# Kernel tuning notes

Measured on AMD Instinct MI355X. Metric: run time of the kernel, lower is better.

The kernel has to match this reference:

```python
import jax, jax.numpy as jnp
import numpy as np

N, C, O, R, T, V = 128, 64, 64, 8, 128, 25  # batch, in_ch, out_ch, rel_ch, frames, joints
EPS = 1e-5


def _c1(x, w, b):
    # 1x1 conv2d over channel dim: x [n,i,t,v], w [o,i], b [o]
    return jnp.einsum('oi,nitv->notv', w, x) + b[None, :, None, None]


def _tconv(x, w):
    # temporal conv, kernel [3,1], pad [1,0]: x [n,c,t,1], w [o,i,3,1]
    return jax.lax.conv_general_dilated(
        x, w, window_strides=(1, 1), padding=((1, 1), (0, 0)),
        dimension_numbers=('NCHW', 'OIHW', 'NCHW'))


def setup_inputs() -> dict:
    key = jax.random.key(0)
    ks = jax.random.split(key, 16)
    d = {}
    d['x'] = jax.random.normal(ks[0], (N, C, T, V), jnp.float32)
    d['A'] = jax.random.normal(ks[1], (V, V), jnp.float32) * 0.1
    d['alpha'] = jnp.ones((1,), jnp.float32)
    s_c = 1.0 / np.sqrt(C)
    s_r = 1.0 / np.sqrt(R)
    d['w1'] = jax.random.normal(ks[2], (R, C), jnp.float32) * s_c
    d['b1'] = jnp.zeros((R,), jnp.float32)
    d['w2'] = jax.random.normal(ks[3], (R, C), jnp.float32) * s_c
    d['b2'] = jnp.zeros((R,), jnp.float32)
    d['w5'] = jax.random.normal(ks[4], (R, C), jnp.float32) * s_c
    d['b5'] = jnp.zeros((R,), jnp.float32)
    d['w3'] = jax.random.normal(ks[5], (O, R), jnp.float32) * s_r
    d['b3'] = jnp.zeros((O,), jnp.float32)
    d['w4'] = jax.random.normal(ks[6], (O, R), jnp.float32) * s_r
    d['b4'] = jnp.zeros((O,), jnp.float32)
    # RouteFuncMLP params (ratio=1, kernels=[3,3])
    d['g_w'] = jax.random.normal(ks[7], (R, R), jnp.float32) * s_r
    d['g_b'] = jnp.zeros((R,), jnp.float32)
    d['a_w'] = jax.random.normal(ks[8], (R, R, 3, 1), jnp.float32) * s_r
    d['a_b'] = jnp.zeros((R,), jnp.float32)
    d['bn_g'] = jnp.ones((R,), jnp.float32)
    d['bn_b'] = jnp.zeros((R,), jnp.float32)
    d['bn_rm'] = jnp.zeros((R,), jnp.float32)
    d['bn_rv'] = jnp.ones((R,), jnp.float32)
    # conv_rf.b is zero-init in torch (trivial gate); randomize small for a meaningful test
    d['rf_bw'] = jax.random.normal(ks[9], (R, R, 3, 1), jnp.float32) * 0.05
    return d


def reference(x, A, alpha, w1, b1, w2, b2, w5, b5, w3, b3, w4, b4,
              g_w, g_b, a_w, a_b, bn_g, bn_b, bn_rm, bn_rv, rf_bw):
    # x1, x2: 1x1 conv then mean over T  -> [N,R,V]
    x1 = _c1(x, w1, b1).mean(axis=2)
    x2 = _c1(x, w2, b2).mean(axis=2)
    x3 = _c1(x, w5, b5)  # [N,R,T,V]

    # RouteFuncMLP gating on x3
    g = x3.mean(axis=(2, 3), keepdims=True)          # global pool [N,R,1,1]
    p = x3.mean(axis=3, keepdims=True)               # pool over V [N,R,T,1]
    gg = _c1(g, g_w, g_b)                            # 1x1 conv on global pool
    h = _tconv(p + gg, a_w) + a_b[None, :, None, None]
    h = (h - bn_rm[None, :, None, None]) * (bn_g / jnp.sqrt(bn_rv + EPS))[None, :, None, None] + bn_b[None, :, None, None]
    h = jax.nn.relu(h)
    rf = _tconv(h, rf_bw) + 1.0                      # [N,R,T,1]

    x3 = _c1(x3 * rf, w3, b3)                        # [N,O,T,V]

    # relation tensor: broadcast diff + tanh -> [N,R,V,V]
    rel = jnp.tanh(x1[:, :, :, None] - x2[:, :, None, :])
    rel = _c1(rel, w4, b4) * alpha[0] + A[None, None]  # [N,O,V,V]

    # aggregation: out[n,c,t,u] = sum_v rel[n,c,u,v] * x3[n,c,t,v]
    out = jnp.einsum('ncuv,nctv->nctu', rel, x3)
    return out
```

## Files before the change

kernel.cpp:

```cpp
#include <hip/hip_runtime.h>

#define N_ 128
#define C_ 64
#define O_ 64
#define R_ 8
#define T_ 128
#define V_ 25
#define TV_ 3200
#define EPS_ 1e-5f
#define G_ 8

__global__ __launch_bounds__(256) void k1_colsum(const float* __restrict__ x,
                                                 float* __restrict__ S) {
    int ni = blockIdx.x;
    const float* xp = x + (size_t)ni * TV_;
    int tid = threadIdx.x;
    __shared__ float part[200];
    if (tid < 200) {
        float s = 0.f;
        #pragma unroll
        for (int k = 0; k < 16; ++k) s += xp[tid + 200 * k];
        part[tid] = s;
    }
    __syncthreads();
    if (tid < V_) {
        float t = 0.f;
        #pragma unroll
        for (int g = 0; g < 8; ++g) t += part[g * 25 + tid];
        S[ni * V_ + tid] = t;
    }
}

__global__ __launch_bounds__(256) void k3_x3(const float* __restrict__ x,
        const float* __restrict__ w5, const float* __restrict__ b5,
        float* __restrict__ x3) {
    int gid = blockIdx.x * 256 + threadIdx.x;
    int n = gid / TV_, p = gid % TV_;
    float acc[R_];
    #pragma unroll
    for (int r = 0; r < R_; ++r) acc[r] = b5[r];
    const float* xp = x + (size_t)n * C_ * TV_ + p;
    #pragma unroll
    for (int i = 0; i < C_; ++i) {
        float xv = xp[(size_t)i * TV_];
        #pragma unroll
        for (int r = 0; r < R_; ++r) acc[r] += w5[r * C_ + i] * xv;
    }
    float* x3p = x3 + (size_t)n * R_ * TV_ + p;
    #pragma unroll
    for (int r = 0; r < R_; ++r) x3p[(size_t)r * TV_] = acc[r];
}

__global__ __launch_bounds__(256) void k2_rel(const float* __restrict__ S,
        const float* __restrict__ w1, const float* __restrict__ b1,
        const float* __restrict__ w2, const float* __restrict__ b2,
        const float* __restrict__ w4, const float* __restrict__ b4,
        const float* __restrict__ A, const float* __restrict__ alpha,
        float* __restrict__ rel2) {
    int n = blockIdx.x, og = blockIdx.y;
    int c0 = og * 16;
    int tid = threadIdx.x;
    __shared__ float x1s[R_ * V_];
    __shared__ float x2s[R_ * V_];
    __shared__ float rels[R_ * 625];
    const float invT = 1.0f / (float)T_;
    for (int idx = tid; idx < 2 * R_ * V_; idx += 256) {
        int s = idx / (R_ * V_), rv = idx % (R_ * V_);
        int r = rv / V_, v = rv % V_;
        const float* w = s ? w2 : w1;
        float a = 0.f;
        for (int i = 0; i < C_; ++i) a += w[r * C_ + i] * S[(n * C_ + i) * V_ + v];
        a = a * invT + (s ? b2[r] : b1[r]);
        (s ? x2s : x1s)[rv] = a;
    }
    __syncthreads();
    for (int idx = tid; idx < R_ * 625; idx += 256) {
        int r = idx / 625, uv = idx % 625;
        rels[idx] = tanhf(x1s[r * V_ + uv / V_] - x2s[r * V_ + uv % V_]);
    }
    __syncthreads();
    float al = alpha[0];
    for (int idx = tid; idx < 16 * 625; idx += 256) {
        int o = c0 + idx / 625, uv = idx % 625;
        float acc = b4[o];
        #pragma unroll
        for (int r = 0; r < R_; ++r) acc += w4[o * R_ + r] * rels[r * 625 + uv];
        rel2[((size_t)n * O_ + o) * 625 + uv] = acc * al + A[uv];
    }
}

__global__ __launch_bounds__(256) void k4_route(const float* __restrict__ x3,
        const float* __restrict__ g_w, const float* __restrict__ g_b,
        const float* __restrict__ a_w, const float* __restrict__ a_b,
        const float* __restrict__ bn_g, const float* __restrict__ bn_b,
        const float* __restrict__ bn_rm, const float* __restrict__ bn_rv,
        const float* __restrict__ rf_bw, float* __restrict__ rf) {
    int n = blockIdx.x, tid = threadIdx.x;
    __shared__ float ps[R_][T_];
    __shared__ float hs[R_][T_];
    __shared__ float gs[R_];
    __shared__ float ggs[R_];
    for (int idx = tid; idx < R_ * T_; idx += 256) {
        int r = idx / T_, t = idx % T_;
        const float* xp = x3 + ((size_t)n * R_ + r) * TV_ + t * V_;
        float s = 0.f;
        #pragma unroll
        for (int v = 0; v < V_; ++v) s += xp[v];
        ps[r][t] = s * (1.0f / V_);
    }
    __syncthreads();
    if (tid < R_) {
        float s = 0.f;
        for (int t = 0; t < T_; ++t) s += ps[tid][t];
        gs[tid] = s * (1.0f / T_);
    }
    __syncthreads();
    if (tid < R_) {
        float a = g_b[tid];
        #pragma unroll
        for (int i = 0; i < R_; ++i) a += g_w[tid * R_ + i] * gs[i];
        ggs[tid] = a;
    }
    __syncthreads();
    for (int idx = tid; idx < R_ * T_; idx += 256) {
        int r = idx / T_, t = idx % T_;
        float acc = a_b[r];
        #pragma unroll
        for (int i = 0; i < R_; ++i) {
            #pragma unroll
            for (int k = 0; k < 3; ++k) {
                int tt = t + k - 1;
                if (tt >= 0 && tt < T_)
                    acc += a_w[(r * R_ + i) * 3 + k] * (ps[i][tt] + ggs[i]);
            }
        }
        float sc = bn_g[r] * rsqrtf(bn_rv[r] + EPS_);
        float h = (acc - bn_rm[r]) * sc + bn_b[r];
        hs[r][t] = fmaxf(h, 0.f);
    }
    __syncthreads();
    for (int idx = tid; idx < R_ * T_; idx += 256) {
        int r = idx / T_, t = idx % T_;
        float acc = 1.0f;
        #pragma unroll
        for (int i = 0; i < R_; ++i) {
            #pragma unroll
            for (int k = 0; k < 3; ++k) {
                int tt = t + k - 1;
                if (tt >= 0 && tt < T_)
                    acc += rf_bw[(r * R_ + i) * 3 + k] * hs[i][tt];
            }
        }
        rf[((size_t)n * R_ + r) * T_ + t] = acc;
    }
}

__global__ __launch_bounds__(512) void k5_out(const float* __restrict__ x3,
        const float* __restrict__ rf, const float* __restrict__ rel2,
        const float* __restrict__ w3, const float* __restrict__ b3,
        float* __restrict__ out) {
    int b = blockIdx.x;
    int n = b / 16;
    int rem = b % 16;
    int cg = rem / 2, th = rem % 2;
    int c0 = cg * G_;
    int tid = threadIdx.x;
    __shared__ float rfs[R_][64];
    __shared__ float zs[G_][1600];
    __shared__ float rels[G_][V_][28];
    if (tid < R_ * 64) {
        int r = tid / 64, tl = tid % 64;
        rfs[r][tl] = rf[((size_t)n * R_ + r) * T_ + th * 64 + tl];
    }
    for (int idx = tid; idx < G_ * 625; idx += 512) {
        int cl = idx / 625, uv = idx % 625;
        rels[cl][uv / 25][uv % 25] = rel2[((size_t)n * O_ + c0 + cl) * 625 + uv];
    }
    __syncthreads();
    const float* x3p = x3 + (size_t)n * R_ * TV_ + th * 1600;
    for (int p = tid; p < 1600; p += 512) {
        int t = p / V_;
        float y[R_];
        #pragma unroll
        for (int r = 0; r < R_; ++r) y[r] = x3p[(size_t)r * TV_ + p] * rfs[r][t];
        #pragma unroll
        for (int cl = 0; cl < G_; ++cl) {
            float a = b3[c0 + cl];
            #pragma unroll
            for (int r = 0; r < R_; ++r) a += w3[(c0 + cl) * R_ + r] * y[r];
            zs[cl][p] = a;
        }
    }
    __syncthreads();
    {
        int cl = tid >> 6, tl = tid & 63;
        float zreg[V_];
        #pragma unroll
        for (int v = 0; v < V_; ++v) zreg[v] = zs[cl][tl * V_ + v];
        float accu[V_];
        #pragma unroll
        for (int u = 0; u < V_; ++u) {
            const float4* rp4 = (const float4*)&rels[cl][u][0];
            float4 a0 = rp4[0], a1 = rp4[1], a2 = rp4[2];
            float4 a3 = rp4[3], a4 = rp4[4], a5 = rp4[5];
            float acc = zreg[24] * rels[cl][u][24];
            acc += zreg[0] * a0.x + zreg[1] * a0.y + zreg[2] * a0.z + zreg[3] * a0.w;
            acc += zreg[4] * a1.x + zreg[5] * a1.y + zreg[6] * a1.z + zreg[7] * a1.w;
            acc += zreg[8] * a2.x + zreg[9] * a2.y + zreg[10] * a2.z + zreg[11] * a2.w;
            acc += zreg[12] * a3.x + zreg[13] * a3.y + zreg[14] * a3.z + zreg[15] * a3.w;
            acc += zreg[16] * a4.x + zreg[17] * a4.y + zreg[18] * a4.z + zreg[19] * a4.w;
            acc += zreg[20] * a5.x + zreg[21] * a5.y + zreg[22] * a5.z + zreg[23] * a5.w;
            accu[u] = acc;
        }
        #pragma unroll
        for (int u = 0; u < V_; ++u) zs[cl][tl * V_ + u] = accu[u];
    }
    __syncthreads();
    size_t ob = (((size_t)n * O_ + c0) * T_ + th * 64) * V_;
    const float* zf = &zs[0][0];
    for (int j = tid; j < G_ * 1600; j += 512) {
        int cl = j / 1600, rest = j % 1600;
        out[ob + (size_t)cl * (T_ * V_) + rest] = zf[j];
    }
}

extern "C" void kernel_launch(void* const* d_in, const int* in_sizes, int n_in,
                              void* d_out, int out_size, void* d_ws, size_t ws_size,
                              hipStream_t stream) {
    const float* x     = (const float*)d_in[0];
    const float* A     = (const float*)d_in[1];
    const float* alpha = (const float*)d_in[2];
    const float* w1    = (const float*)d_in[3];
    const float* b1    = (const float*)d_in[4];
    const float* w2    = (const float*)d_in[5];
    const float* b2    = (const float*)d_in[6];
    const float* w5    = (const float*)d_in[7];
    const float* b5    = (const float*)d_in[8];
    const float* w3    = (const float*)d_in[9];
    const float* b3    = (const float*)d_in[10];
    const float* w4    = (const float*)d_in[11];
    const float* b4    = (const float*)d_in[12];
    const float* g_w   = (const float*)d_in[13];
    const float* g_b   = (const float*)d_in[14];
    const float* a_w   = (const float*)d_in[15];
    const float* a_b   = (const float*)d_in[16];
    const float* bn_g  = (const float*)d_in[17];
    const float* bn_b  = (const float*)d_in[18];
    const float* bn_rm = (const float*)d_in[19];
    const float* bn_rv = (const float*)d_in[20];
    const float* rf_bw = (const float*)d_in[21];
    float* out = (float*)d_out;
    float* ws  = (float*)d_ws;

    float* S     = ws;
    float* x3    = S + 204800;
    float* rf    = x3 + 3276800;
    float* rel2  = rf + 131072;

    hipLaunchKernelGGL(k1_colsum, dim3(N_ * C_), dim3(256), 0, stream, x, S);
    hipLaunchKernelGGL(k3_x3, dim3(1600), dim3(256), 0, stream, x, w5, b5, x3);
    hipLaunchKernelGGL(k2_rel, dim3(N_, 4), dim3(256), 0, stream,
                       S, w1, b1, w2, b2, w4, b4, A, alpha, rel2);
    hipLaunchKernelGGL(k4_route, dim3(N_), dim3(256), 0, stream,
                       x3, g_w, g_b, a_w, a_b, bn_g, bn_b, bn_rm, bn_rv, rf_bw, rf);
    hipLaunchKernelGGL(k5_out, dim3(N_ * 16), dim3(512), 0, stream,
                       x3, rf, rel2, w3, b3, out);
}
```

Baseline: 322.7 us.

## Split route pooling into parallel kernel and read rel from global in output kernel

The V-pooling of x3 moves out of the route kernel into a new kernel with one block per (n,r), using coalesced loads staged in shared memory. The route kernel is split over two time halves with halo recomputation, so more blocks run. The output kernel no longer stages rel into shared memory; each wave reads rel2 directly through a wave-uniform pointer, and the final store is vectorised to float4. The cost is an extra launch, a pooled-buffer round trip, and possibly slower uncached global reads of rel inside the inner loop.

```diff
diff --git a/kernel.cpp b/kernel.cpp
--- a/kernel.cpp
+++ b/kernel.cpp
@@ -89,66 +89,82 @@
     }
 }
 
-__global__ __launch_bounds__(256) void k4_route(const float* __restrict__ x3,
+__global__ __launch_bounds__(256) void kP_pool(const float* __restrict__ x3,
+                                               float* __restrict__ ppool) {
+    int nr = blockIdx.x;
+    int tid = threadIdx.x;
+    __shared__ float buf[TV_];
+    const float* xp = x3 + (size_t)nr * TV_;
+    for (int idx = tid; idx < TV_; idx += 256) buf[idx] = xp[idx];
+    __syncthreads();
+    if (tid < T_) {
+        float s = 0.f;
+        #pragma unroll
+        for (int v = 0; v < V_; ++v) s += buf[tid * V_ + v];
+        ppool[(size_t)nr * T_ + tid] = s;
+    }
+}
+
+__global__ __launch_bounds__(256) void k4b_route(const float* __restrict__ ppool,
         const float* __restrict__ g_w, const float* __restrict__ g_b,
         const float* __restrict__ a_w, const float* __restrict__ a_b,
         const float* __restrict__ bn_g, const float* __restrict__ bn_b,
         const float* __restrict__ bn_rm, const float* __restrict__ bn_rv,
         const float* __restrict__ rf_bw, float* __restrict__ rf) {
-    int n = blockIdx.x, tid = threadIdx.x;
+    int n = blockIdx.x, th = blockIdx.y;
+    int t0 = th * 64;
+    int tid = threadIdx.x;
     __shared__ float ps[R_][T_];
-    __shared__ float hs[R_][T_];
-    __shared__ float gs[R_];
+    __shared__ float hs[R_][68];
     __shared__ float ggs[R_];
-    for (int idx = tid; idx < R_ * T_; idx += 256) {
-        int r = idx / T_, t = idx % T_;
-        const float* xp = x3 + ((size_t)n * R_ + r) * TV_ + t * V_;
-        float s = 0.f;
-        #pragma unroll
-        for (int v = 0; v < V_; ++v) s += xp[v];
-        ps[r][t] = s * (1.0f / V_);
-    }
+    for (int idx = tid; idx < R_ * T_; idx += 256)
+        ps[idx / T_][idx % T_] = ppool[(size_t)n * R_ * T_ + idx] * (1.0f / V_);
     __syncthreads();
     if (tid < R_) {
         float s = 0.f;
         for (int t = 0; t < T_; ++t) s += ps[tid][t];
-        gs[tid] = s * (1.0f / T_);
+        hs[tid][0] = s * (1.0f / T_);
     }
     __syncthreads();
     if (tid < R_) {
         float a = g_b[tid];
         #pragma unroll
-        for (int i = 0; i < R_; ++i) a += g_w[tid * R_ + i] * gs[i];
+        for (int i = 0; i < R_; ++i) a += g_w[tid * R_ + i] * hs[i][0];
         ggs[tid] = a;
     }
     __syncthreads();
-    for (int idx = tid; idx < R_ * T_; idx += 256) {
-        int r = idx / T_, t = idx % T_;
-        float acc = a_b[r];
+    for (int idx = tid; idx < R_ * 66; idx += 256) {
+        int r = idx / 66, j = idx % 66;
+        int t = t0 + j - 1;
+        float h = 0.f;
+        if (t >= 0 && t < T_) {
+            float acc = a_b[r];
+            #pragma unroll
+            for (int i = 0; i < R_; ++i) {
+                #pragma unroll
+                for (int k = 0; k < 3; ++k) {
+                    int tt = t + k - 1;
+                    if (tt >= 0 && tt < T_)
+                        acc += a_w[(r * R_ + i) * 3 + k] * (ps[i][tt] + ggs[i]);
+                }
+            }
+            float sc = bn_g[r] * rsqrtf(bn_rv[r] + EPS_);
+            h = fmaxf((acc - bn_rm[r]) * sc + bn_b[r], 0.f);
+        }
+        hs[r][j + 1] = h;
+    }
+    __syncthreads();
+    for (int idx = tid; idx < R_ * 64; idx += 256) {
+        int r = idx / 64, j = idx % 64;
+        int t = t0 + j;
+        float acc = 1.0f;
         #pragma unroll
         for (int i = 0; i < R_; ++i) {
             #pragma unroll
             for (int k = 0; k < 3; ++k) {
                 int tt = t + k - 1;
                 if (tt >= 0 && tt < T_)
-                    acc += a_w[(r * R_ + i) * 3 + k] * (ps[i][tt] + ggs[i]);
-            }
-        }
-        float sc = bn_g[r] * rsqrtf(bn_rv[r] + EPS_);
-        float h = (acc - bn_rm[r]) * sc + bn_b[r];
-        hs[r][t] = fmaxf(h, 0.f);
-    }
-    __syncthreads();
-    for (int idx = tid; idx < R_ * T_; idx += 256) {
-        int r = idx / T_, t = idx % T_;
-        float acc = 1.0f;
-        #pragma unroll
-        for (int i = 0; i < R_; ++i) {
-            #pragma unroll
-            for (int k = 0; k < 3; ++k) {
-                int tt = t + k - 1;
-                if (tt >= 0 && tt < T_)
-                    acc += rf_bw[(r * R_ + i) * 3 + k] * hs[i][tt];
+                    acc += rf_bw[(r * R_ + i) * 3 + k] * hs[i][j + k + 1];
             }
         }
         rf[((size_t)n * R_ + r) * T_ + t] = acc;
@@ -166,15 +182,10 @@
     int c0 = cg * G_;
     int tid = threadIdx.x;
     __shared__ float rfs[R_][64];
-    __shared__ float zs[G_][1600];
-    __shared__ float rels[G_][V_][28];
-    if (tid < R_ * 64) {
+    __shared__ __align__(16) float zs[G_][1600];
+    {
         int r = tid / 64, tl = tid % 64;
         rfs[r][tl] = rf[((size_t)n * R_ + r) * T_ + th * 64 + tl];
-    }
-    for (int idx = tid; idx < G_ * 625; idx += 512) {
-        int cl = idx / 625, uv = idx % 625;
-        rels[cl][uv / 25][uv % 25] = rel2[((size_t)n * O_ + c0 + cl) * 625 + uv];
     }
     __syncthreads();
     const float* x3p = x3 + (size_t)n * R_ * TV_ + th * 1600;
@@ -193,23 +204,18 @@
     }
     __syncthreads();
     {
-        int cl = tid >> 6, tl = tid & 63;
+        int cl = __builtin_amdgcn_readfirstlane(tid >> 6);
+        int tl = tid & 63;
+        const float* relp = rel2 + ((size_t)n * O_ + c0 + cl) * 625;
         float zreg[V_];
         #pragma unroll
         for (int v = 0; v < V_; ++v) zreg[v] = zs[cl][tl * V_ + v];
         float accu[V_];
         #pragma unroll
         for (int u = 0; u < V_; ++u) {
-            const float4* rp4 = (const float4*)&rels[cl][u][0];
-            float4 a0 = rp4[0], a1 = rp4[1], a2 = rp4[2];
-            float4 a3 = rp4[3], a4 = rp4[4], a5 = rp4[5];
-            float acc = zreg[24] * rels[cl][u][24];
-            acc += zreg[0] * a0.x + zreg[1] * a0.y + zreg[2] * a0.z + zreg[3] * a0.w;
-            acc += zreg[4] * a1.x + zreg[5] * a1.y + zreg[6] * a1.z + zreg[7] * a1.w;
-            acc += zreg[8] * a2.x + zreg[9] * a2.y + zreg[10] * a2.z + zreg[11] * a2.w;
-            acc += zreg[12] * a3.x + zreg[13] * a3.y + zreg[14] * a3.z + zreg[15] * a3.w;
-            acc += zreg[16] * a4.x + zreg[17] * a4.y + zreg[18] * a4.z + zreg[19] * a4.w;
-            acc += zreg[20] * a5.x + zreg[21] * a5.y + zreg[22] * a5.z + zreg[23] * a5.w;
+            float acc = 0.f;
+            #pragma unroll
+            for (int j = 0; j < V_; ++j) acc += relp[u * V_ + j] * zreg[j];
             accu[u] = acc;
         }
         #pragma unroll
@@ -217,10 +223,11 @@
     }
     __syncthreads();
     size_t ob = (((size_t)n * O_ + c0) * T_ + th * 64) * V_;
-    const float* zf = &zs[0][0];
-    for (int j = tid; j < G_ * 1600; j += 512) {
-        int cl = j / 1600, rest = j % 1600;
-        out[ob + (size_t)cl * (T_ * V_) + rest] = zf[j];
+    float4* out4 = (float4*)(out + ob);
+    const float4* zf4 = (const float4*)&zs[0][0];
+    for (int j = tid; j < 3200; j += 512) {
+        int cl = j / 400, r4 = j % 400;
+        out4[(size_t)cl * 800 + r4] = zf4[j];
     }
 }
 
@@ -254,15 +261,17 @@
 
     float* S     = ws;
     float* x3    = S + 204800;
-    float* rf    = x3 + 3276800;
+    float* ppool = x3 + 3276800;
+    float* rf    = ppool + 131072;
     float* rel2  = rf + 131072;
 
     hipLaunchKernelGGL(k1_colsum, dim3(N_ * C_), dim3(256), 0, stream, x, S);
     hipLaunchKernelGGL(k3_x3, dim3(1600), dim3(256), 0, stream, x, w5, b5, x3);
     hipLaunchKernelGGL(k2_rel, dim3(N_, 4), dim3(256), 0, stream,
                        S, w1, b1, w2, b2, w4, b4, A, alpha, rel2);
-    hipLaunchKernelGGL(k4_route, dim3(N_), dim3(256), 0, stream,
-                       x3, g_w, g_b, a_w, a_b, bn_g, bn_b, bn_rm, bn_rv, rf_bw, rf);
+    hipLaunchKernelGGL(kP_pool, dim3(N_ * R_), dim3(256), 0, stream, x3, ppool);
+    hipLaunchKernelGGL(k4b_route, dim3(N_, 2), dim3(256), 0, stream,
+                       ppool, g_w, g_b, a_w, a_b, bn_g, bn_b, bn_rm, bn_rv, rf_bw, rf);
     hipLaunchKernelGGL(k5_out, dim3(N_ * 16), dim3(512), 0, stream,
                        x3, rf, rel2, w3, b3, out);
 }
```

Measured after the change: 318.0 us. Within noise of the previous version (-1.5%).
